# Kernel optimization log

Measured on AMD Instinct MI355X. Metric: run time of the kernel, lower is better.

## Reference

```python
import jax, jax.numpy as jnp
import numpy as np

N = 1024      # n_nodes
S = 32        # state_dim
M = 32        # message_dim
STEPS = 5     # n_steps


def setup_inputs() -> dict:
    key = jax.random.key(0)
    ks = jax.random.split(key, 12)
    w = lambda k, shape: jax.random.normal(k, shape, jnp.float32) * 0.02
    return {
        "J": jax.random.normal(ks[0], (N, N), jnp.float32),
        "b": jax.random.normal(ks[1], (N,), jnp.float32),
        # message_passing MLP (Linear(2S+3->M), Linear(M->M), Linear(M->M))
        "W1": w(ks[2], (M, 2 * S + 3)), "b1": jnp.zeros((M,), jnp.float32),
        "W2": w(ks[3], (M, M)),         "b2": jnp.zeros((M,), jnp.float32),
        "W3": w(ks[4], (M, M)),         "b3": jnp.zeros((M,), jnp.float32),
        # GRU(input=S+M, hidden=S). h0 is always zero in the original forward,
        # so weight_hh never contributes (only bias_hh does) and is omitted.
        "W_ih": w(ks[5], (3 * S, S + M)),
        "b_ih": w(ks[6], (3 * S,)),
        "b_hh": w(ks[7], (3 * S,)),
        # readout MLP (Linear(S->M), Linear(M->M), Linear(M->2))
        "R1": w(ks[8], (M, S)),  "rb1": jnp.zeros((M,), jnp.float32),
        "R2": w(ks[9], (M, M)),  "rb2": jnp.zeros((M,), jnp.float32),
        "R3": w(ks[10], (2, M)), "rb3": jnp.zeros((2,), jnp.float32),
    }


def reference(J, b, W1, b1, W2, b2, W3, b3, W_ih, b_ih, b_hh, R1, rb1, R2, rb2, R3, rb3):
    # Split first linear over the concat [h_i, h_j, J_ij, b_i, b_j] so the
    # [N, N, 2S+3] concat tensor is never materialized.
    W1a, W1b = W1[:, :S], W1[:, S:2 * S]
    wJ, wbi, wbj = W1[:, 2 * S], W1[:, 2 * S + 1], W1[:, 2 * S + 2]

    def step(h, _):
        hi = h @ W1a.T                       # [N, M] (sender part)
        hj = h @ W1b.T                       # [N, M] (receiver part)
        pre = (hi[:, None, :] + hj[None, :, :]
               + J[:, :, None] * wJ
               + b[:, None, None] * wbi
               + b[None, :, None] * wbj
               + b1)                          # [N, N, M]
        x = jax.nn.relu(pre)
        x = jax.nn.relu(x @ W2.T + b2)
        x = jax.nn.relu(x @ W3.T + b3)       # message_i_j: [N, N, M]
        m = x.sum(0)                          # message to node j: sum over senders i
        # GRU with zero initial hidden state: h' = (1-z) * n_gate
        gi = jnp.concatenate([h, m], axis=-1) @ W_ih.T + b_ih  # [N, 3S]
        r = jax.nn.sigmoid(gi[:, :S] + b_hh[:S])
        z = jax.nn.sigmoid(gi[:, S:2 * S] + b_hh[S:2 * S])
        n = jnp.tanh(gi[:, 2 * S:] + r * b_hh[2 * S:])
        return (1.0 - z) * n, None

    h0 = jnp.zeros((N, S), J.dtype)
    h, _ = jax.lax.scan(step, h0, None, length=STEPS)

    r = jax.nn.relu(h @ R1.T + rb1)
    r = jax.nn.relu(r @ R2.T + rb2)
    r = jax.nn.relu(r @ R3.T + rb3)          # [N, 2]
    return jax.nn.sigmoid(r)
```

## Files before the change

### kernel.cpp

```cpp
#include <hip/hip_runtime.h>
#include <hip/hip_bf16.h>
#include <math.h>

#define NN 1024

typedef __attribute__((ext_vector_type(8))) short bf16x8;
typedef __attribute__((ext_vector_type(4))) float f32x4;
typedef __attribute__((ext_vector_type(4))) unsigned int u32x4;

__device__ __forceinline__ float sigmoidf_(float x) { return 1.0f / (1.0f + __expf(-x)); }

__device__ __forceinline__ unsigned short f2bf(float x) {
    __hip_bfloat16 h = __float2bfloat16(x);
    return *reinterpret_cast<unsigned short*>(&h);
}
__device__ __forceinline__ unsigned int pack2(unsigned short a, unsigned short b) {
    return (unsigned int)a | ((unsigned int)b << 16);
}

__global__ __launch_bounds__(256) void k_init(
    const float* __restrict__ b, const float* __restrict__ W1,
    const float* __restrict__ b1, float* __restrict__ h,
    float* __restrict__ mbuf, float* __restrict__ u, float* __restrict__ v)
{
    int t = blockIdx.x * 256 + threadIdx.x;
    int row = t >> 5;
    int mm  = t & 31;
    float bi = b[row];
    h[t]    = 0.0f;
    mbuf[t] = 0.0f;
    u[t] = bi * W1[mm * 67 + 65];
    v[t] = fmaf(bi, W1[mm * 67 + 66], b1[mm]);
}

__global__ __launch_bounds__(256) void k_tr(
    const float* __restrict__ J, float* __restrict__ Jt)
{
    __shared__ float tile[32][33];
    int bx = blockIdx.x * 32, by = blockIdx.y * 32;
    int x = threadIdx.x, y = threadIdx.y;
#pragma unroll
    for (int r = 0; r < 4; r++)
        tile[y + 8 * r][x] = J[(by + y + 8 * r) * NN + bx + x];
    __syncthreads();
#pragma unroll
    for (int r = 0; r < 4; r++)
        Jt[(bx + y + 8 * r) * NN + by + x] = tile[x][y + 8 * r];
}

__global__ __launch_bounds__(256) void k_main(
    const float* __restrict__ J, const float* __restrict__ Jt, int useJt,
    const float* __restrict__ W1,
    const float* __restrict__ W2, const float* __restrict__ b2,
    const float* __restrict__ W3, const float* __restrict__ b3,
    const float* __restrict__ u,  const float* __restrict__ v,
    float* __restrict__ mout)
{
    __shared__ unsigned int ybuf[4 * 640];
    __shared__ float red[4 * 32];

    const int tid = threadIdx.x;
    const int w = tid >> 6;
    const int l = tid & 63;
    const int p = l & 15;
    const int q = l >> 4;
    const int j = blockIdx.x;

    union FU { bf16x8 v; unsigned short s[8]; } w2a0, w2a1, w3a0, w3a1;
#pragma unroll
    for (int jj = 0; jj < 8; jj++) {
        int k = q * 8 + jj;
        w2a0.s[jj] = f2bf(W2[p * 32 + k]);
        w2a1.s[jj] = f2bf(W2[(16 + p) * 32 + k]);
        w3a0.s[jj] = f2bf(W3[p * 32 + k]);
        w3a1.s[jj] = f2bf(W3[(16 + p) * 32 + k]);
    }
    float vv[8], wj8[8];
#pragma unroll
    for (int jj = 0; jj < 8; jj++) {
        int k = q * 8 + jj;
        vv[jj]  = v[j * 32 + k];
        wj8[jj] = W1[k * 67 + 64];
    }
    float b2v0[4], b2v1[4], b3v0[4], b3v1[4];
#pragma unroll
    for (int r = 0; r < 4; r++) {
        b2v0[r] = b2[q * 4 + r];  b2v1[r] = b2[16 + q * 4 + r];
        b3v0[r] = b3[q * 4 + r];  b3v1[r] = b3[16 + q * 4 + r];
    }

    const f32x4 zero = {0.f, 0.f, 0.f, 0.f};
    f32x4 acc0 = zero, acc1 = zero;

    const float* __restrict__ jptr = useJt ? (Jt + (size_t)j * NN) : (J + j);
    const int jstride = useJt ? 1 : NN;
    const int ibase = w * 256;

#pragma unroll 2
    for (int t = 0; t < 16; ++t) {
        const int i = ibase + t * 16 + p;
        const float jw = jptr[(size_t)i * jstride];
        const float4 u0 = *(const float4*)(u + i * 32 + q * 8);
        const float4 u1 = *(const float4*)(u + i * 32 + q * 8 + 4);
        float xk[8];
        xk[0] = u0.x; xk[1] = u0.y; xk[2] = u0.z; xk[3] = u0.w;
        xk[4] = u1.x; xk[5] = u1.y; xk[6] = u1.z; xk[7] = u1.w;

        union FU bx;
#pragma unroll
        for (int jj = 0; jj < 8; jj++) {
            float t2 = fmaf(jw, wj8[jj], xk[jj] + vv[jj]);
            bx.s[jj] = f2bf(fmaxf(t2, 0.f));
        }

        f32x4 c0 = __builtin_amdgcn_mfma_f32_16x16x32_bf16(w2a0.v, bx.v, zero, 0, 0, 0);
        f32x4 c1 = __builtin_amdgcn_mfma_f32_16x16x32_bf16(w2a1.v, bx.v, zero, 0, 0, 0);

        unsigned int* yb = ybuf + w * 640 + (t & 1) * 320;
        unsigned int d0 = pack2(f2bf(fmaxf(c0[0] + b2v0[0], 0.f)),
                                f2bf(fmaxf(c0[1] + b2v0[1], 0.f)));
        unsigned int d1 = pack2(f2bf(fmaxf(c0[2] + b2v0[2], 0.f)),
                                f2bf(fmaxf(c0[3] + b2v0[3], 0.f)));
        unsigned int d2 = pack2(f2bf(fmaxf(c1[0] + b2v1[0], 0.f)),
                                f2bf(fmaxf(c1[1] + b2v1[1], 0.f)));
        unsigned int d3 = pack2(f2bf(fmaxf(c1[2] + b2v1[2], 0.f)),
                                f2bf(fmaxf(c1[3] + b2v1[3], 0.f)));
        yb[p * 20 + q * 2 + 0] = d0;
        yb[p * 20 + q * 2 + 1] = d1;
        yb[p * 20 + 8 + q * 2 + 0] = d2;
        yb[p * 20 + 8 + q * 2 + 1] = d3;

        union { u32x4 u4; bf16x8 v; } yrd;
        yrd.u4 = *(const u32x4*)(yb + p * 20 + q * 4);

        f32x4 e0 = __builtin_amdgcn_mfma_f32_16x16x32_bf16(w3a0.v, yrd.v, zero, 0, 0, 0);
        f32x4 e1 = __builtin_amdgcn_mfma_f32_16x16x32_bf16(w3a1.v, yrd.v, zero, 0, 0, 0);
#pragma unroll
        for (int r = 0; r < 4; r++) {
            acc0[r] += fmaxf(e0[r] + b3v0[r], 0.f);
            acc1[r] += fmaxf(e1[r] + b3v1[r], 0.f);
        }
    }

#pragma unroll
    for (int bit = 1; bit < 16; bit <<= 1) {
#pragma unroll
        for (int r = 0; r < 4; r++) {
            acc0[r] += __shfl_xor(acc0[r], bit);
            acc1[r] += __shfl_xor(acc1[r], bit);
        }
    }
    if (p == 0) {
#pragma unroll
        for (int r = 0; r < 4; r++) {
            red[w * 32 + q * 4 + r]      = acc0[r];
            red[w * 32 + 16 + q * 4 + r] = acc1[r];
        }
    }
    __syncthreads();
    if (tid < 32) {
        float s = red[tid] + red[32 + tid] + red[64 + tid] + red[96 + tid];
        mout[j * 32 + tid] = s;
    }
}

__global__ __launch_bounds__(256) void k_gru(
    const float* __restrict__ Wih, const float* __restrict__ bih,
    const float* __restrict__ bhh, const float* __restrict__ W1,
    const float* __restrict__ b,   const float* __restrict__ b1,
    float* __restrict__ h, float* __restrict__ mbuf,
    float* __restrict__ u, float* __restrict__ v)
{
    const int tid = threadIdx.x;
    const int s = tid & 31;
    const int j = blockIdx.x * 8 + (tid >> 5);

    const float hval = h[j * 32 + s];
    const float mval = mbuf[j * 32 + s];

    float g0 = bih[s];
    float g1 = bih[32 + s];
    float g2 = bih[64 + s];
#pragma unroll
    for (int k = 0; k < 32; k++) {
        float hk = __shfl(hval, k, 32);
        float mk = __shfl(mval, k, 32);
        g0 = fmaf(Wih[s * 64 + k],        hk, g0);
        g0 = fmaf(Wih[s * 64 + 32 + k],   mk, g0);
        g1 = fmaf(Wih[(32 + s) * 64 + k],      hk, g1);
        g1 = fmaf(Wih[(32 + s) * 64 + 32 + k], mk, g1);
        g2 = fmaf(Wih[(64 + s) * 64 + k],      hk, g2);
        g2 = fmaf(Wih[(64 + s) * 64 + 32 + k], mk, g2);
    }
    float r = sigmoidf_(g0 + bhh[s]);
    float z = sigmoidf_(g1 + bhh[32 + s]);
    float n = tanhf(g2 + r * bhh[64 + s]);
    float hn = (1.0f - z) * n;
    h[j * 32 + s] = hn;

    float bj = b[j];
    float uacc = bj * W1[s * 67 + 65];
    float vacc = fmaf(bj, W1[s * 67 + 66], b1[s]);
#pragma unroll
    for (int k = 0; k < 32; k++) {
        float hk = __shfl(hn, k, 32);
        uacc = fmaf(W1[s * 67 + k],      hk, uacc);
        vacc = fmaf(W1[s * 67 + 32 + k], hk, vacc);
    }
    u[j * 32 + s] = uacc;
    v[j * 32 + s] = vacc;
}

__global__ __launch_bounds__(256) void k_out(
    const float* __restrict__ h,
    const float* __restrict__ R1, const float* __restrict__ rb1,
    const float* __restrict__ R2, const float* __restrict__ rb2,
    const float* __restrict__ R3, const float* __restrict__ rb3,
    float* __restrict__ out)
{
    const int tid = threadIdx.x;
    const int s = tid & 31;
    const int j = blockIdx.x * 8 + (tid >> 5);

    float hv = h[j * 32 + s];
    float a1 = rb1[s];
#pragma unroll
    for (int k = 0; k < 32; k++) a1 = fmaf(R1[s * 32 + k], __shfl(hv, k, 32), a1);
    a1 = fmaxf(a1, 0.0f);

    float a2 = rb2[s];
#pragma unroll
    for (int k = 0; k < 32; k++) a2 = fmaf(R2[s * 32 + k], __shfl(a1, k, 32), a2);
    a2 = fmaxf(a2, 0.0f);

    float acc3 = 0.0f;
#pragma unroll
    for (int k = 0; k < 32; k++) {
        float a2k = __shfl(a2, k, 32);
        if (s < 2) acc3 = fmaf(R3[s * 32 + k], a2k, acc3);
    }
    if (s < 2) {
        float r3 = fmaxf(acc3 + rb3[s], 0.0f);
        out[j * 2 + s] = sigmoidf_(r3);
    }
}

extern "C" void kernel_launch(void* const* d_in, const int* in_sizes, int n_in,
                              void* d_out, int out_size, void* d_ws, size_t ws_size,
                              hipStream_t stream)
{
    const float* J   = (const float*)d_in[0];
    const float* b   = (const float*)d_in[1];
    const float* W1  = (const float*)d_in[2];
    const float* b1  = (const float*)d_in[3];
    const float* W2  = (const float*)d_in[4];
    const float* b2  = (const float*)d_in[5];
    const float* W3  = (const float*)d_in[6];
    const float* b3  = (const float*)d_in[7];
    const float* Wih = (const float*)d_in[8];
    const float* bih = (const float*)d_in[9];
    const float* bhh = (const float*)d_in[10];
    const float* R1  = (const float*)d_in[11];
    const float* rb1 = (const float*)d_in[12];
    const float* R2  = (const float*)d_in[13];
    const float* rb2 = (const float*)d_in[14];
    const float* R3  = (const float*)d_in[15];
    const float* rb3 = (const float*)d_in[16];

    float* out = (float*)d_out;
    float* ws  = (float*)d_ws;
    float* h  = ws;
    float* mb = ws + 32768;
    float* u  = ws + 65536;
    float* v  = ws + 98304;
    float* Jt = ws + 131072;

    const size_t need = (131072 + (size_t)NN * NN) * sizeof(float);
    const int useJt = (ws_size >= need) ? 1 : 0;

    k_init<<<128, 256, 0, stream>>>(b, W1, b1, h, mb, u, v);
    if (useJt) k_tr<<<dim3(32, 32), dim3(32, 8), 0, stream>>>(J, Jt);
    for (int step = 0; step < 5; ++step) {
        k_main<<<1024, 256, 0, stream>>>(J, Jt, useJt, W1, W2, b2, W3, b3, u, v, mb);
        k_gru<<<128, 256, 0, stream>>>(Wih, bih, bhh, W1, b, b1, h, mb, u, v);
    }
    k_out<<<128, 256, 0, stream>>>(h, R1, rb1, R2, rb2, R3, rb3, out);
}
```

Measured before the change: 247.1 us.

## Fuse message, GRU and readout into one cooperative persistent kernel

Merges the five message/GRU step pairs and the readout into a single cooperative kernel of 1024 blocks with 128 threads each. Steps are separated by grid-wide syncs, and h and v stay in shared memory. Transpose and init are folded into one pre-kernel. Biases go into the MFMA accumulator inputs, and a bit-trick bf16 pack replaces the library conversion. This cuts roughly ten kernel launches and the global round trips for m, h and v, at the cost of grid-barrier overhead and half as many threads per block. A fallback of five fused step kernels runs when cooperative launch is not possible, and the path without a transposed J is dropped.

```diff
diff --git a/kernel.cpp b/kernel.cpp
--- a/kernel.cpp
+++ b/kernel.cpp
@@ -1,6 +1,8 @@
 #include <hip/hip_runtime.h>
-#include <hip/hip_bf16.h>
+#include <hip/hip_cooperative_groups.h>
 #include <math.h>
+
+namespace cg = cooperative_groups;
 
 #define NN 1024
 
@@ -10,54 +12,189 @@
 
 __device__ __forceinline__ float sigmoidf_(float x) { return 1.0f / (1.0f + __expf(-x)); }
 
-__device__ __forceinline__ unsigned short f2bf(float x) {
-    __hip_bfloat16 h = __float2bfloat16(x);
-    return *reinterpret_cast<unsigned short*>(&h);
-}
-__device__ __forceinline__ unsigned int pack2(unsigned short a, unsigned short b) {
-    return (unsigned int)a | ((unsigned int)b << 16);
-}
-
-__global__ __launch_bounds__(256) void k_init(
-    const float* __restrict__ b, const float* __restrict__ W1,
-    const float* __restrict__ b1, float* __restrict__ h,
-    float* __restrict__ mbuf, float* __restrict__ u, float* __restrict__ v)
-{
-    int t = blockIdx.x * 256 + threadIdx.x;
-    int row = t >> 5;
-    int mm  = t & 31;
-    float bi = b[row];
-    h[t]    = 0.0f;
-    mbuf[t] = 0.0f;
-    u[t] = bi * W1[mm * 67 + 65];
-    v[t] = fmaf(bi, W1[mm * 67 + 66], b1[mm]);
-}
-
-__global__ __launch_bounds__(256) void k_tr(
-    const float* __restrict__ J, float* __restrict__ Jt)
+__device__ __forceinline__ unsigned int pk_bf16(float a, float b) {
+    unsigned int ua = __float_as_uint(a), ub = __float_as_uint(b);
+    ua += 0x7fffu + ((ua >> 16) & 1u);
+    ub += 0x7fffu + ((ub >> 16) & 1u);
+    return (ua >> 16) | (ub & 0xffff0000u);
+}
+__device__ __forceinline__ unsigned short f2bf_rne(float a) {
+    unsigned int ua = __float_as_uint(a);
+    ua += 0x7fffu + ((ua >> 16) & 1u);
+    return (unsigned short)(ua >> 16);
+}
+
+struct Ctx {
+    bf16x8 w2a0, w2a1, w3a0, w3a1;
+    f32x4 b2v0, b2v1, b3v0, b3v1;
+    float wj8[8];
+};
+
+__device__ __forceinline__ void make_ctx(Ctx& c, int p, int q,
+    const float* __restrict__ W1, const float* __restrict__ W2,
+    const float* __restrict__ b2, const float* __restrict__ W3,
+    const float* __restrict__ b3)
+{
+    union FU { bf16x8 v; unsigned short s[8]; } t0, t1, t2, t3;
+#pragma unroll
+    for (int jj = 0; jj < 8; jj++) {
+        int k = q * 8 + jj;
+        t0.s[jj] = f2bf_rne(W2[p * 32 + k]);
+        t1.s[jj] = f2bf_rne(W2[(16 + p) * 32 + k]);
+        t2.s[jj] = f2bf_rne(W3[p * 32 + k]);
+        t3.s[jj] = f2bf_rne(W3[(16 + p) * 32 + k]);
+        c.wj8[jj] = W1[k * 67 + 64];
+    }
+    c.w2a0 = t0.v; c.w2a1 = t1.v; c.w3a0 = t2.v; c.w3a1 = t3.v;
+#pragma unroll
+    for (int r = 0; r < 4; r++) {
+        c.b2v0[r] = b2[q * 4 + r];  c.b2v1[r] = b2[16 + q * 4 + r];
+        c.b3v0[r] = b3[q * 4 + r];  c.b3v1[r] = b3[16 + q * 4 + r];
+    }
+}
+
+__device__ __forceinline__ void tile_op(const Ctx& c,
+    const float* __restrict__ Jtrow, const float* __restrict__ u,
+    const float* vv, unsigned int* yb, int i, int p, int q,
+    f32x4& acc0, f32x4& acc1)
+{
+    const float jw = Jtrow[i];
+    const float4 u0 = *(const float4*)(u + i * 32 + q * 8);
+    const float4 u1 = *(const float4*)(u + i * 32 + q * 8 + 4);
+    float xr[8];
+    xr[0] = fmaxf(fmaf(jw, c.wj8[0], u0.x + vv[0]), 0.f);
+    xr[1] = fmaxf(fmaf(jw, c.wj8[1], u0.y + vv[1]), 0.f);
+    xr[2] = fmaxf(fmaf(jw, c.wj8[2], u0.z + vv[2]), 0.f);
+    xr[3] = fmaxf(fmaf(jw, c.wj8[3], u0.w + vv[3]), 0.f);
+    xr[4] = fmaxf(fmaf(jw, c.wj8[4], u1.x + vv[4]), 0.f);
+    xr[5] = fmaxf(fmaf(jw, c.wj8[5], u1.y + vv[5]), 0.f);
+    xr[6] = fmaxf(fmaf(jw, c.wj8[6], u1.z + vv[6]), 0.f);
+    xr[7] = fmaxf(fmaf(jw, c.wj8[7], u1.w + vv[7]), 0.f);
+
+    union BU { u32x4 u4; bf16x8 v; unsigned int d[4]; } bx;
+#pragma unroll
+    for (int cc = 0; cc < 4; cc++) bx.d[cc] = pk_bf16(xr[2 * cc], xr[2 * cc + 1]);
+
+    f32x4 c0 = __builtin_amdgcn_mfma_f32_16x16x32_bf16(c.w2a0, bx.v, c.b2v0, 0, 0, 0);
+    f32x4 c1 = __builtin_amdgcn_mfma_f32_16x16x32_bf16(c.w2a1, bx.v, c.b2v1, 0, 0, 0);
+
+    yb[p * 20 + q * 2 + 0]     = pk_bf16(fmaxf(c0[0], 0.f), fmaxf(c0[1], 0.f));
+    yb[p * 20 + q * 2 + 1]     = pk_bf16(fmaxf(c0[2], 0.f), fmaxf(c0[3], 0.f));
+    yb[p * 20 + 8 + q * 2 + 0] = pk_bf16(fmaxf(c1[0], 0.f), fmaxf(c1[1], 0.f));
+    yb[p * 20 + 8 + q * 2 + 1] = pk_bf16(fmaxf(c1[2], 0.f), fmaxf(c1[3], 0.f));
+
+    union BU yrd;
+    yrd.u4 = *(const u32x4*)(yb + p * 20 + q * 4);
+
+    f32x4 e0 = __builtin_amdgcn_mfma_f32_16x16x32_bf16(c.w3a0, yrd.v, c.b3v0, 0, 0, 0);
+    f32x4 e1 = __builtin_amdgcn_mfma_f32_16x16x32_bf16(c.w3a1, yrd.v, c.b3v1, 0, 0, 0);
+#pragma unroll
+    for (int r = 0; r < 4; r++) {
+        acc0[r] += fmaxf(e0[r], 0.f);
+        acc1[r] += fmaxf(e1[r], 0.f);
+    }
+}
+
+__device__ __forceinline__ void gru_row(int s, float hval, float mval, float bj,
+    const float* __restrict__ Wih, const float* __restrict__ bih,
+    const float* __restrict__ bhh, const float* __restrict__ W1,
+    const float* __restrict__ b1, float& hn, float& uacc, float& vacc)
+{
+    float g0 = bih[s], g1 = bih[32 + s], g2 = bih[64 + s];
+#pragma unroll 8
+    for (int k = 0; k < 32; k++) {
+        float hk = __shfl(hval, k, 32);
+        float mk = __shfl(mval, k, 32);
+        g0 = fmaf(Wih[s * 64 + k],             hk, g0);
+        g0 = fmaf(Wih[s * 64 + 32 + k],        mk, g0);
+        g1 = fmaf(Wih[(32 + s) * 64 + k],      hk, g1);
+        g1 = fmaf(Wih[(32 + s) * 64 + 32 + k], mk, g1);
+        g2 = fmaf(Wih[(64 + s) * 64 + k],      hk, g2);
+        g2 = fmaf(Wih[(64 + s) * 64 + 32 + k], mk, g2);
+    }
+    float r = sigmoidf_(g0 + bhh[s]);
+    float z = sigmoidf_(g1 + bhh[32 + s]);
+    float n = tanhf(g2 + r * bhh[64 + s]);
+    hn = (1.0f - z) * n;
+    float ua = bj * W1[s * 67 + 65];
+    float va = fmaf(bj, W1[s * 67 + 66], b1[s]);
+#pragma unroll 8
+    for (int k = 0; k < 32; k++) {
+        float hk = __shfl(hn, k, 32);
+        ua = fmaf(W1[s * 67 + k],      hk, ua);
+        va = fmaf(W1[s * 67 + 32 + k], hk, va);
+    }
+    uacc = ua; vacc = va;
+}
+
+__device__ __forceinline__ void readout_row(int s, int j, float hn,
+    const float* __restrict__ R1, const float* __restrict__ rb1,
+    const float* __restrict__ R2, const float* __restrict__ rb2,
+    const float* __restrict__ R3, const float* __restrict__ rb3,
+    float* __restrict__ out)
+{
+    float a1 = rb1[s];
+#pragma unroll 8
+    for (int k = 0; k < 32; k++) a1 = fmaf(R1[s * 32 + k], __shfl(hn, k, 32), a1);
+    a1 = fmaxf(a1, 0.f);
+    float a2 = rb2[s];
+#pragma unroll 8
+    for (int k = 0; k < 32; k++) a2 = fmaf(R2[s * 32 + k], __shfl(a1, k, 32), a2);
+    a2 = fmaxf(a2, 0.f);
+    float a3 = (s < 2) ? rb3[s] : 0.f;
+#pragma unroll 8
+    for (int k = 0; k < 32; k++) {
+        float a2k = __shfl(a2, k, 32);
+        if (s < 2) a3 = fmaf(R3[s * 32 + k], a2k, a3);
+    }
+    if (s < 2) out[j * 2 + s] = sigmoidf_(fmaxf(a3, 0.f));
+}
+
+__global__ __launch_bounds__(256) void k_pre(
+    const float* __restrict__ J, const float* __restrict__ b,
+    const float* __restrict__ W1, const float* __restrict__ b1,
+    float* __restrict__ Jt, float* __restrict__ h,
+    float* __restrict__ u0, float* __restrict__ v)
 {
     __shared__ float tile[32][33];
-    int bx = blockIdx.x * 32, by = blockIdx.y * 32;
-    int x = threadIdx.x, y = threadIdx.y;
-#pragma unroll
-    for (int r = 0; r < 4; r++)
-        tile[y + 8 * r][x] = J[(by + y + 8 * r) * NN + bx + x];
-    __syncthreads();
-#pragma unroll
-    for (int r = 0; r < 4; r++)
-        Jt[(bx + y + 8 * r) * NN + by + x] = tile[x][y + 8 * r];
-}
-
-__global__ __launch_bounds__(256) void k_main(
-    const float* __restrict__ J, const float* __restrict__ Jt, int useJt,
-    const float* __restrict__ W1,
+    const int t = blockIdx.x;
+    const int tid = threadIdx.x;
+    if (t < 1024) {
+        int tx = (t & 31) * 32, ty = (t >> 5) * 32;
+        int x = tid & 31, y = tid >> 5;
+#pragma unroll
+        for (int r = 0; r < 4; r++)
+            tile[y + 8 * r][x] = J[(size_t)(ty + y + 8 * r) * NN + tx + x];
+        __syncthreads();
+#pragma unroll
+        for (int r = 0; r < 4; r++)
+            Jt[(size_t)(tx + y + 8 * r) * NN + ty + x] = tile[x][y + 8 * r];
+    } else {
+        int idx = (t - 1024) * 256 + tid;
+        int row = idx >> 5, mm = idx & 31;
+        float bi = b[row];
+        h[idx]  = 0.f;
+        u0[idx] = bi * W1[mm * 67 + 65];
+        v[idx]  = fmaf(bi, W1[mm * 67 + 66], b1[mm]);
+    }
+}
+
+__global__ __launch_bounds__(128, 2) void k_coop(
+    const float* __restrict__ Jt, const float* __restrict__ W1,
     const float* __restrict__ W2, const float* __restrict__ b2,
     const float* __restrict__ W3, const float* __restrict__ b3,
-    const float* __restrict__ u,  const float* __restrict__ v,
-    float* __restrict__ mout)
-{
-    __shared__ unsigned int ybuf[4 * 640];
-    __shared__ float red[4 * 32];
+    const float* __restrict__ Wih, const float* __restrict__ bih,
+    const float* __restrict__ bhh, const float* __restrict__ b,
+    const float* __restrict__ b1,
+    const float* __restrict__ R1, const float* __restrict__ rb1,
+    const float* __restrict__ R2, const float* __restrict__ rb2,
+    const float* __restrict__ R3, const float* __restrict__ rb3,
+    const float* __restrict__ vin, float* __restrict__ u0,
+    float* __restrict__ u1, float* __restrict__ out)
+{
+    __shared__ unsigned int ybuf[2 * 4 * 320];
+    __shared__ float red[2 * 32];
+    __shared__ float hbuf[32], vbuf[32];
 
     const int tid = threadIdx.x;
     const int w = tid >> 6;
@@ -66,81 +203,92 @@
     const int q = l >> 4;
     const int j = blockIdx.x;
 
-    union FU { bf16x8 v; unsigned short s[8]; } w2a0, w2a1, w3a0, w3a1;
-#pragma unroll
-    for (int jj = 0; jj < 8; jj++) {
-        int k = q * 8 + jj;
-        w2a0.s[jj] = f2bf(W2[p * 32 + k]);
-        w2a1.s[jj] = f2bf(W2[(16 + p) * 32 + k]);
-        w3a0.s[jj] = f2bf(W3[p * 32 + k]);
-        w3a1.s[jj] = f2bf(W3[(16 + p) * 32 + k]);
-    }
-    float vv[8], wj8[8];
-#pragma unroll
-    for (int jj = 0; jj < 8; jj++) {
-        int k = q * 8 + jj;
-        vv[jj]  = v[j * 32 + k];
-        wj8[jj] = W1[k * 67 + 64];
-    }
-    float b2v0[4], b2v1[4], b3v0[4], b3v1[4];
-#pragma unroll
-    for (int r = 0; r < 4; r++) {
-        b2v0[r] = b2[q * 4 + r];  b2v1[r] = b2[16 + q * 4 + r];
-        b3v0[r] = b3[q * 4 + r];  b3v1[r] = b3[16 + q * 4 + r];
-    }
-
-    const f32x4 zero = {0.f, 0.f, 0.f, 0.f};
-    f32x4 acc0 = zero, acc1 = zero;
-
-    const float* __restrict__ jptr = useJt ? (Jt + (size_t)j * NN) : (J + j);
-    const int jstride = useJt ? 1 : NN;
-    const int ibase = w * 256;
-
+    Ctx c; make_ctx(c, p, q, W1, W2, b2, W3, b3);
+    const float* Jtrow = Jt + (size_t)j * NN;
+
+    if (tid < 32) { hbuf[tid] = 0.f; vbuf[tid] = vin[j * 32 + tid]; }
+    __syncthreads();
+
+    for (int step = 0; step < 5; ++step) {
+        const float* ui = (step & 1) ? u1 : u0;
+        float*       uo = (step & 1) ? u0 : u1;
+
+        float vv[8];
+#pragma unroll
+        for (int jj = 0; jj < 8; jj++) vv[jj] = vbuf[q * 8 + jj];
+
+        f32x4 acc0 = {0.f, 0.f, 0.f, 0.f}, acc1 = {0.f, 0.f, 0.f, 0.f};
+#pragma unroll 4
+        for (int t = 0; t < 32; ++t)
+            tile_op(c, Jtrow, ui, vv, ybuf + w * 1280 + (t & 3) * 320,
+                    w * 512 + t * 16 + p, p, q, acc0, acc1);
+
+#pragma unroll
+        for (int bit = 1; bit < 16; bit <<= 1) {
+#pragma unroll
+            for (int r = 0; r < 4; r++) {
+                acc0[r] += __shfl_xor(acc0[r], bit);
+                acc1[r] += __shfl_xor(acc1[r], bit);
+            }
+        }
+        if (p == 0) {
+#pragma unroll
+            for (int r = 0; r < 4; r++) {
+                red[w * 32 + q * 4 + r]      = acc0[r];
+                red[w * 32 + 16 + q * 4 + r] = acc1[r];
+            }
+        }
+        __syncthreads();
+
+        if (tid < 32) {
+            const int s = tid;
+            float mval = red[s] + red[32 + s];
+            float hn, ua, va;
+            gru_row(s, hbuf[s], mval, b[j], Wih, bih, bhh, W1, b1, hn, ua, va);
+            hbuf[s] = hn; vbuf[s] = va;
+            uo[j * 32 + s] = ua;
+            if (step == 4) readout_row(s, j, hn, R1, rb1, R2, rb2, R3, rb3, out);
+        }
+        if (step < 4) { __threadfence(); cg::this_grid().sync(); }
+    }
+}
+
+__global__ __launch_bounds__(256, 4) void k_step(
+    const float* __restrict__ Jt, const float* __restrict__ W1,
+    const float* __restrict__ W2, const float* __restrict__ b2,
+    const float* __restrict__ W3, const float* __restrict__ b3,
+    const float* __restrict__ Wih, const float* __restrict__ bih,
+    const float* __restrict__ bhh, const float* __restrict__ b,
+    const float* __restrict__ b1,
+    const float* __restrict__ R1, const float* __restrict__ rb1,
+    const float* __restrict__ R2, const float* __restrict__ rb2,
+    const float* __restrict__ R3, const float* __restrict__ rb3,
+    float* __restrict__ h, float* __restrict__ v,
+    const float* __restrict__ ui, float* __restrict__ uo,
+    float* __restrict__ out, int do_out)
+{
+    __shared__ unsigned int ybuf[4 * 2 * 320];
+    __shared__ float red[4 * 32];
+
+    const int tid = threadIdx.x;
+    const int w = tid >> 6;
+    const int l = tid & 63;
+    const int p = l & 15;
+    const int q = l >> 4;
+    const int j = blockIdx.x;
+
+    Ctx c; make_ctx(c, p, q, W1, W2, b2, W3, b3);
+    const float* Jtrow = Jt + (size_t)j * NN;
+
+    float vv[8];
+#pragma unroll
+    for (int jj = 0; jj < 8; jj++) vv[jj] = v[j * 32 + q * 8 + jj];
+
+    f32x4 acc0 = {0.f, 0.f, 0.f, 0.f}, acc1 = {0.f, 0.f, 0.f, 0.f};
 #pragma unroll 2
-    for (int t = 0; t < 16; ++t) {
-        const int i = ibase + t * 16 + p;
-        const float jw = jptr[(size_t)i * jstride];
-        const float4 u0 = *(const float4*)(u + i * 32 + q * 8);
-        const float4 u1 = *(const float4*)(u + i * 32 + q * 8 + 4);
-        float xk[8];
-        xk[0] = u0.x; xk[1] = u0.y; xk[2] = u0.z; xk[3] = u0.w;
-        xk[4] = u1.x; xk[5] = u1.y; xk[6] = u1.z; xk[7] = u1.w;
-
-        union FU bx;
-#pragma unroll
-        for (int jj = 0; jj < 8; jj++) {
-            float t2 = fmaf(jw, wj8[jj], xk[jj] + vv[jj]);
-            bx.s[jj] = f2bf(fmaxf(t2, 0.f));
-        }
-
-        f32x4 c0 = __builtin_amdgcn_mfma_f32_16x16x32_bf16(w2a0.v, bx.v, zero, 0, 0, 0);
-        f32x4 c1 = __builtin_amdgcn_mfma_f32_16x16x32_bf16(w2a1.v, bx.v, zero, 0, 0, 0);
-
-        unsigned int* yb = ybuf + w * 640 + (t & 1) * 320;
-        unsigned int d0 = pack2(f2bf(fmaxf(c0[0] + b2v0[0], 0.f)),
-                                f2bf(fmaxf(c0[1] + b2v0[1], 0.f)));
-        unsigned int d1 = pack2(f2bf(fmaxf(c0[2] + b2v0[2], 0.f)),
-                                f2bf(fmaxf(c0[3] + b2v0[3], 0.f)));
-        unsigned int d2 = pack2(f2bf(fmaxf(c1[0] + b2v1[0], 0.f)),
-                                f2bf(fmaxf(c1[1] + b2v1[1], 0.f)));
-        unsigned int d3 = pack2(f2bf(fmaxf(c1[2] + b2v1[2], 0.f)),
-                                f2bf(fmaxf(c1[3] + b2v1[3], 0.f)));
-        yb[p * 20 + q * 2 + 0] = d0;
-        yb[p * 20 + q * 2 + 1] = d1;
-        yb[p * 20 + 8 + q * 2 + 0] = d2;
-        yb[p * 20 + 8 + q * 2 + 1] = d3;
-
-        union { u32x4 u4; bf16x8 v; } yrd;
-        yrd.u4 = *(const u32x4*)(yb + p * 20 + q * 4);
-
-        f32x4 e0 = __builtin_amdgcn_mfma_f32_16x16x32_bf16(w3a0.v, yrd.v, zero, 0, 0, 0);
-        f32x4 e1 = __builtin_amdgcn_mfma_f32_16x16x32_bf16(w3a1.v, yrd.v, zero, 0, 0, 0);
-#pragma unroll
-        for (int r = 0; r < 4; r++) {
-            acc0[r] += fmaxf(e0[r] + b3v0[r], 0.f);
-            acc1[r] += fmaxf(e1[r] + b3v1[r], 0.f);
-        }
-    }
+    for (int t = 0; t < 16; ++t)
+        tile_op(c, Jtrow, ui, vv, ybuf + w * 640 + (t & 1) * 320,
+                w * 256 + t * 16 + p, p, q, acc0, acc1);
 
 #pragma unroll
     for (int bit = 1; bit < 16; bit <<= 1) {
@@ -158,90 +306,16 @@
         }
     }
     __syncthreads();
+
     if (tid < 32) {
-        float s = red[tid] + red[32 + tid] + red[64 + tid] + red[96 + tid];
-        mout[j * 32 + tid] = s;
-    }
-}
-
-__global__ __launch_bounds__(256) void k_gru(
-    const float* __restrict__ Wih, const float* __restrict__ bih,
-    const float* __restrict__ bhh, const float* __restrict__ W1,
-    const float* __restrict__ b,   const float* __restrict__ b1,
-    float* __restrict__ h, float* __restrict__ mbuf,
-    float* __restrict__ u, float* __restrict__ v)
-{
-    const int tid = threadIdx.x;
-    const int s = tid & 31;
-    const int j = blockIdx.x * 8 + (tid >> 5);
-
-    const float hval = h[j * 32 + s];
-    const float mval = mbuf[j * 32 + s];
-
-    float g0 = bih[s];
-    float g1 = bih[32 + s];
-    float g2 = bih[64 + s];
-#pragma unroll
-    for (int k = 0; k < 32; k++) {
-        float hk = __shfl(hval, k, 32);
-        float mk = __shfl(mval, k, 32);
-        g0 = fmaf(Wih[s * 64 + k],        hk, g0);
-        g0 = fmaf(Wih[s * 64 + 32 + k],   mk, g0);
-        g1 = fmaf(Wih[(32 + s) * 64 + k],      hk, g1);
-        g1 = fmaf(Wih[(32 + s) * 64 + 32 + k], mk, g1);
-        g2 = fmaf(Wih[(64 + s) * 64 + k],      hk, g2);
-        g2 = fmaf(Wih[(64 + s) * 64 + 32 + k], mk, g2);
-    }
-    float r = sigmoidf_(g0 + bhh[s]);
-    float z = sigmoidf_(g1 + bhh[32 + s]);
-    float n = tanhf(g2 + r * bhh[64 + s]);
-    float hn = (1.0f - z) * n;
-    h[j * 32 + s] = hn;
-
-    float bj = b[j];
-    float uacc = bj * W1[s * 67 + 65];
-    float vacc = fmaf(bj, W1[s * 67 + 66], b1[s]);
-#pragma unroll
-    for (int k = 0; k < 32; k++) {
-        float hk = __shfl(hn, k, 32);
-        uacc = fmaf(W1[s * 67 + k],      hk, uacc);
-        vacc = fmaf(W1[s * 67 + 32 + k], hk, vacc);
-    }
-    u[j * 32 + s] = uacc;
-    v[j * 32 + s] = vacc;
-}
-
-__global__ __launch_bounds__(256) void k_out(
-    const float* __restrict__ h,
-    const float* __restrict__ R1, const float* __restrict__ rb1,
-    const float* __restrict__ R2, const float* __restrict__ rb2,
-    const float* __restrict__ R3, const float* __restrict__ rb3,
-    float* __restrict__ out)
-{
-    const int tid = threadIdx.x;
-    const int s = tid & 31;
-    const int j = blockIdx.x * 8 + (tid >> 5);
-
-    float hv = h[j * 32 + s];
-    float a1 = rb1[s];
-#pragma unroll
-    for (int k = 0; k < 32; k++) a1 = fmaf(R1[s * 32 + k], __shfl(hv, k, 32), a1);
-    a1 = fmaxf(a1, 0.0f);
-
-    float a2 = rb2[s];
-#pragma unroll
-    for (int k = 0; k < 32; k++) a2 = fmaf(R2[s * 32 + k], __shfl(a1, k, 32), a2);
-    a2 = fmaxf(a2, 0.0f);
-
-    float acc3 = 0.0f;
-#pragma unroll
-    for (int k = 0; k < 32; k++) {
-        float a2k = __shfl(a2, k, 32);
-        if (s < 2) acc3 = fmaf(R3[s * 32 + k], a2k, acc3);
-    }
-    if (s < 2) {
-        float r3 = fmaxf(acc3 + rb3[s], 0.0f);
-        out[j * 2 + s] = sigmoidf_(r3);
+        const int s = tid;
+        float mval = red[s] + red[32 + s] + red[64 + s] + red[96 + s];
+        float hn, ua, va;
+        gru_row(s, h[j * 32 + s], mval, b[j], Wih, bih, bhh, W1, b1, hn, ua, va);
+        h[j * 32 + s] = hn;
+        v[j * 32 + s] = va;
+        uo[j * 32 + s] = ua;
+        if (do_out) readout_row(s, j, hn, R1, rb1, R2, rb2, R3, rb3, out);
     }
 }
 
@@ -270,19 +344,39 @@
     float* out = (float*)d_out;
     float* ws  = (float*)d_ws;
     float* h  = ws;
-    float* mb = ws + 32768;
-    float* u  = ws + 65536;
-    float* v  = ws + 98304;
+    float* v  = ws + 32768;
+    float* u0 = ws + 65536;
+    float* u1 = ws + 98304;
     float* Jt = ws + 131072;
 
-    const size_t need = (131072 + (size_t)NN * NN) * sizeof(float);
-    const int useJt = (ws_size >= need) ? 1 : 0;
-
-    k_init<<<128, 256, 0, stream>>>(b, W1, b1, h, mb, u, v);
-    if (useJt) k_tr<<<dim3(32, 32), dim3(32, 8), 0, stream>>>(J, Jt);
-    for (int step = 0; step < 5; ++step) {
-        k_main<<<1024, 256, 0, stream>>>(J, Jt, useJt, W1, W2, b2, W3, b3, u, v, mb);
-        k_gru<<<128, 256, 0, stream>>>(Wih, bih, bhh, W1, b, b1, h, mb, u, v);
-    }
-    k_out<<<128, 256, 0, stream>>>(h, R1, rb1, R2, rb2, R3, rb3, out);
-}
+    k_pre<<<1152, 256, 0, stream>>>(J, b, W1, b1, Jt, h, u0, v);
+
+    int mb = 0;
+    bool coop =
+        (hipOccupancyMaxActiveBlocksPerMultiprocessor(
+             &mb, reinterpret_cast<const void*>(&k_coop), 128, 0) == hipSuccess) &&
+        (mb >= 4);
+    if (coop) {
+        const float* vin = v;
+        void* cargs[] = { (void*)&Jt, (void*)&W1, (void*)&W2, (void*)&b2,
+                          (void*)&W3, (void*)&b3, (void*)&Wih, (void*)&bih,
+                          (void*)&bhh, (void*)&b, (void*)&b1,
+                          (void*)&R1, (void*)&rb1, (void*)&R2, (void*)&rb2,
+                          (void*)&R3, (void*)&rb3,
+                          (void*)&vin, (void*)&u0, (void*)&u1, (void*)&out };
+        if (hipLaunchCooperativeKernel(reinterpret_cast<const void*>(&k_coop),
+                                       dim3(1024), dim3(128), cargs, 0, stream)
+            != hipSuccess)
+            coop = false;
+    }
+    if (!coop) {
+        for (int s = 0; s < 5; s++) {
+            const float* ui = (s & 1) ? u1 : u0;
+            float*       uo = (s & 1) ? u0 : u1;
+            k_step<<<1024, 256, 0, stream>>>(Jt, W1, W2, b2, W3, b3, Wih, bih,
+                                             bhh, b, b1, R1, rb1, R2, rb2, R3,
+                                             rb3, h, v, ui, uo, out,
+                                             (s == 4) ? 1 : 0);
+        }
+    }
+}
```

Result: faster. 224.5 us (-9.2%).
